# Kernel optimization log

Hardware: AMD Instinct MI355X
Metric: run time of the kernel (lower is better)

## Reference

```python
import jax, jax.numpy as jnp
import numpy as np

N = 32768        # nodes
E = 524288       # edges (avg degree 16)
F_NODE = 64      # NODE_FEATURE_DIM
H = 128          # GNN_HIDDEN
F_EDGE = 32      # EDGE_FEATURE_DIM
L = 3            # GNN_LAYERS
D = 256          # D_MODEL
B = 64           # graphs per batch
MAXN = N // B    # 512 nodes per graph (equal-size for static to_dense_batch)


def setup_inputs() -> dict:
    key = jax.random.key(0)
    ks = jax.random.split(key, 10)
    p = lambda k, shape: jax.random.normal(k, shape, jnp.float32) * 0.02
    return {
        "x": jax.random.normal(ks[0], (N, F_NODE), jnp.float32),
        "edge_attr": jax.random.normal(ks[1], (E, F_EDGE), jnp.float32),
        "node_emb_w": p(ks[2], (F_NODE, H)), "node_emb_b": jnp.zeros((H,), jnp.float32),
        "msg_w1": p(ks[3], (L, 2 * H + F_EDGE, 2 * H)), "msg_b1": jnp.zeros((L, 2 * H), jnp.float32),
        "msg_w2": p(ks[4], (L, 2 * H, H)), "msg_b2": jnp.zeros((L, H), jnp.float32),
        "upd_w": p(ks[5], (L, 2 * H, H)), "upd_b": jnp.zeros((L, H), jnp.float32),
        "upd_ln_g": jnp.ones((L, H), jnp.float32), "upd_ln_b": jnp.zeros((L, H), jnp.float32),
        "norm_g": jnp.ones((L, H), jnp.float32), "norm_b": jnp.zeros((L, H), jnp.float32),
        "proj_w": p(ks[6], (H, D)), "proj_b": jnp.zeros((D,), jnp.float32),
        "edge_index": jax.random.randint(ks[7], (2, E), 0, N),
        "batch": jnp.arange(N, dtype=jnp.int32) // MAXN,  # sorted, 64 graphs of 512
    }


def layer_norm(x, g, b, eps=1e-5):
    m = x.mean(-1, keepdims=True)
    v = ((x - m) ** 2).mean(-1, keepdims=True)
    return (x - m) * jax.lax.rsqrt(v + eps) * g + b


def reference(x, edge_attr, node_emb_w, node_emb_b, msg_w1, msg_b1, msg_w2, msg_b2,
              upd_w, upd_b, upd_ln_g, upd_ln_b, norm_g, norm_b, proj_w, proj_b,
              edge_index, batch):
    src, dst = edge_index[0], edge_index[1]  # PyG: x_j = x[src], x_i = x[dst]
    h = x @ node_emb_w + node_emb_b          # [N, H]
    n_layers = msg_w1.shape[0]
    for l in range(n_layers):
        # message: gather -> concat -> MLP (dropout inactive at eval)
        m = jnp.concatenate([h[dst], h[src], edge_attr], axis=-1)  # [E, 2H+Fe]
        m = jax.nn.relu(m @ msg_w1[l] + msg_b1[l])
        m = m @ msg_w2[l] + msg_b2[l]                               # [E, H]
        # aggregate: scatter-add over destination nodes
        aggr = jax.ops.segment_sum(m, dst, num_segments=h.shape[0])  # [N, H]
        # update: concat -> Linear -> ReLU -> LayerNorm
        u = jnp.concatenate([h, aggr], axis=-1) @ upd_w[l] + upd_b[l]
        u = layer_norm(jax.nn.relu(u), upd_ln_g[l], upd_ln_b[l])
        # residual + outer LayerNorm
        h = layer_norm(h + u, norm_g[l], norm_b[l])
    # to_dense_batch (batch sorted, equal-size graphs -> static [B, MAXN])
    n = h.shape[0]
    counts = jax.ops.segment_sum(jnp.ones((n,), jnp.int32), batch, num_segments=B)
    starts = jnp.concatenate([jnp.zeros((1,), jnp.int32), jnp.cumsum(counts)[:-1]])
    pos = jnp.arange(n, dtype=jnp.int32) - starts[batch]
    dense = jnp.zeros((B, MAXN, h.shape[-1]), h.dtype).at[batch, pos].set(h)
    mask = jnp.zeros((B, MAXN), bool).at[batch, pos].set(True)
    return dense @ proj_w + proj_b, mask
```

## Files before the change

### kernel.cpp

```cpp
#include <hip/hip_runtime.h>

#define NN 32768
#define NE 524288

typedef __attribute__((ext_vector_type(8))) short bf16x8;
typedef __attribute__((ext_vector_type(4))) float f32x4;

__device__ __forceinline__ unsigned short f2bf(float f) {
  unsigned int u = __float_as_uint(f);
  unsigned int r = (u + 0x7FFFu + ((u >> 16) & 1u)) >> 16;
  return (unsigned short)r;
}
__device__ __forceinline__ float bf2f(unsigned short s) {
  return __uint_as_float(((unsigned int)s) << 16);
}

__device__ __forceinline__ void lds_fence_wave() {
  asm volatile("s_waitcnt lgkmcnt(0)" ::: "memory");
  __builtin_amdgcn_sched_barrier(0);
}

__device__ __forceinline__ void prep_frag_body(
    const float* __restrict__ W, int row0, int ldw, long lstrW,
    unsigned short* __restrict__ out, int outOff, int outLstr,
    int K, int N, int t, int total) {
  if (t >= total) return;
  int lane = t & 63, fi = t >> 6;
  int FR = (K >> 5) * (N >> 4);
  int l = fi / FR; fi -= l * FR;
  int NT = N >> 4;
  int nt = fi % NT, kc = fi / NT;
  int i = lane & 15, g = lane >> 4;
  const float* base = W + (long)l * lstrW;
  bf16x8 v;
#pragma unroll
  for (int j = 0; j < 8; ++j)
    v[j] = (short)f2bf(base[(long)(row0 + kc * 32 + g * 8 + j) * ldw + nt * 16 + i]);
  reinterpret_cast<bf16x8*>(out)[(long)(l * outLstr + outOff + fi) * 64 + lane] = v;
}

__global__ void prep_all_kernel(const float* __restrict__ emb_w,
                                const float* __restrict__ msg_w1,
                                const float* __restrict__ upd_w,
                                const float* __restrict__ wcomp,
                                const float* __restrict__ proj_w,
                                unsigned short* __restrict__ wembf,
                                unsigned short* __restrict__ w1af,
                                unsigned short* __restrict__ w1bf,
                                unsigned short* __restrict__ w1cf,
                                unsigned short* __restrict__ wupdf,
                                unsigned short* __restrict__ wprojf) {
  int b = blockIdx.x, tid = threadIdx.x;
  if (b < 4)        prep_frag_body(emb_w,  0,   128, 0,     wembf,  0,  16, 64,  128, b * 256 + tid, 1024);
  else if (b < 52)  prep_frag_body(msg_w1, 0,   256, 73728, w1af,   0,  64, 128, 256, (b - 4) * 256 + tid, 12288);
  else if (b < 100) prep_frag_body(msg_w1, 128, 256, 73728, w1bf,   0,  64, 128, 256, (b - 52) * 256 + tid, 12288);
  else if (b < 112) prep_frag_body(msg_w1, 256, 256, 73728, w1cf,   0,  16, 32,  256, (b - 100) * 256 + tid, 3072);
  else if (b < 136) prep_frag_body(upd_w,  0,   128, 32768, wupdf,  0,  96, 128, 128, (b - 112) * 256 + tid, 6144);
  else if (b < 184) prep_frag_body(wcomp,  0,   128, 32768, wupdf,  32, 96, 256, 128, (b - 136) * 256 + tid, 12288);
  else              prep_frag_body(proj_w, 0,   256, 0,     wprojf, 0,  64, 128, 256, (b - 184) * 256 + tid, 4096);
}

__global__ void wcomp_kernel(const float* __restrict__ W2, const float* __restrict__ Wu,
                             const float* __restrict__ b2,
                             float* __restrict__ out, float* __restrict__ c2out) {
  int t = blockIdx.x * 256 + threadIdx.x;
  if (t < 3 * 256 * 128) {
    int c = t & 127, a = (t >> 7) & 255, l = t >> 15;
    const float* w2 = W2 + (long)l * 32768 + a * 128;
    const float* wu = Wu + (long)l * 32768 + 128 * 128 + c;
    float s = 0.f;
#pragma unroll 8
    for (int j = 0; j < 128; ++j) s += w2[j] * wu[j * 128];
    out[t] = s;
  } else {
    int t2 = t - 3 * 256 * 128;
    if (t2 < 3 * 128) {
      int c = t2 & 127, l = t2 >> 7;
      const float* bb = b2 + l * 128;
      const float* wu = Wu + (long)l * 32768 + 128 * 128 + c;
      float s = 0.f;
#pragma unroll 8
      for (int j = 0; j < 128; ++j) s += bb[j] * wu[j * 128];
      c2out[t2] = s;
    }
  }
}

__global__ void hist_kernel(const int* __restrict__ eidx, int* __restrict__ deg) {
  int t = blockIdx.x * 256 + threadIdx.x;
  if (t < NE) atomicAdd(&deg[eidx[NE + t]], 1);
}

__global__ void scan_kernel(const int* __restrict__ deg, int* __restrict__ cursor,
                            float* __restrict__ degf) {
  __shared__ int lds[1024];
  int t = threadIdx.x;
  int vals[32];
  int s = 0;
#pragma unroll
  for (int j = 0; j < 32; ++j) {
    int d = deg[t * 32 + j];
    vals[j] = d; s += d;
    degf[t * 32 + j] = (float)d;
  }
  lds[t] = s;
  __syncthreads();
  for (int off = 1; off < 1024; off <<= 1) {
    int tmp = 0;
    if (t >= off) tmp = lds[t - off];
    __syncthreads();
    lds[t] += tmp;
    __syncthreads();
  }
  int run = lds[t] - s;
#pragma unroll
  for (int j = 0; j < 32; ++j) { cursor[t * 32 + j] = run; run += vals[j]; }
}

__global__ void scatter_kernel(const int* __restrict__ eidx, const float* __restrict__ ea,
                               int* __restrict__ cursor,
                               int* __restrict__ dsts, int* __restrict__ srcs,
                               unsigned short* __restrict__ ea_s) {
  int t = blockIdx.x * 256 + threadIdx.x;
  if (t >= NE) return;
  int d = eidx[NE + t], s = eidx[t];
  int pos = atomicAdd(&cursor[d], 1);
  dsts[pos] = d;
  srcs[pos] = s;
  const float4* ep = reinterpret_cast<const float4*>(ea + (long)t * 32);
  unsigned short* op = ea_s + (long)pos * 32;
#pragma unroll
  for (int q = 0; q < 4; ++q) {
    float4 f0 = ep[2 * q], f1 = ep[2 * q + 1];
    bf16x8 v;
    v[0] = (short)f2bf(f0.x); v[1] = (short)f2bf(f0.y);
    v[2] = (short)f2bf(f0.z); v[3] = (short)f2bf(f0.w);
    v[4] = (short)f2bf(f1.x); v[5] = (short)f2bf(f1.y);
    v[6] = (short)f2bf(f1.z); v[7] = (short)f2bf(f1.w);
    *reinterpret_cast<bf16x8*>(op + q * 8) = v;
  }
}

__global__ __launch_bounds__(256, 2)
void node_emb_kernel(const float* __restrict__ x,
                     const unsigned short* __restrict__ wf,
                     const float* __restrict__ bias,
                     unsigned short* __restrict__ h_bf) {
  int tid = threadIdx.x, lane = tid & 63, w = tid >> 6;
  int i = lane & 15, g = lane >> 4;
  int nbase = blockIdx.x * 64 + w * 16;
  f32x4 zero = {0.f, 0.f, 0.f, 0.f};
  f32x4 acc[8];
#pragma unroll
  for (int nt = 0; nt < 8; ++nt) acc[nt] = zero;
#pragma unroll
  for (int kc = 0; kc < 2; ++kc) {
    const float* xp = x + (nbase + i) * 64 + kc * 32 + g * 8;
    float4 f0 = *reinterpret_cast<const float4*>(xp);
    float4 f1 = *reinterpret_cast<const float4*>(xp + 4);
    bf16x8 af;
    af[0] = (short)f2bf(f0.x); af[1] = (short)f2bf(f0.y);
    af[2] = (short)f2bf(f0.z); af[3] = (short)f2bf(f0.w);
    af[4] = (short)f2bf(f1.x); af[5] = (short)f2bf(f1.y);
    af[6] = (short)f2bf(f1.z); af[7] = (short)f2bf(f1.w);
#pragma unroll
    for (int nt = 0; nt < 8; ++nt) {
      bf16x8 bf = reinterpret_cast<const bf16x8*>(wf)[(kc * 8 + nt) * 64 + lane];
      acc[nt] = __builtin_amdgcn_mfma_f32_16x16x32_bf16(af, bf, acc[nt], 0, 0, 0);
    }
  }
#pragma unroll
  for (int nt = 0; nt < 8; ++nt) {
    int c = nt * 16 + i;
    float b = bias[c];
#pragma unroll
    for (int r = 0; r < 4; ++r) {
      int node = nbase + 4 * g + r;
      h_bf[node * 128 + c] = f2bf(acc[nt][r] + b);
    }
  }
}

__global__ __launch_bounds__(256, 2)
void pq_kernel(const unsigned short* __restrict__ h_bf,
               const unsigned short* __restrict__ wfa,
               const unsigned short* __restrict__ wfb,
               const float* __restrict__ b1,
               unsigned short* __restrict__ P, unsigned short* __restrict__ Q,
               float* __restrict__ haggr) {
  __shared__ unsigned short xpose[64 * 264];
  int tid = threadIdx.x, lane = tid & 63, w = tid >> 6;
  int i = lane & 15, g = lane >> 4;
  int nbase = blockIdx.x * 64 + w * 16;
  {
    const float4 zz = make_float4(0.f, 0.f, 0.f, 0.f);
    float4* hz = reinterpret_cast<float4*>(haggr + (long)blockIdx.x * 64 * 256);
#pragma unroll
    for (int it = 0; it < 16; ++it) hz[tid + 256 * it] = zz;
  }
  f32x4 zero = {0.f, 0.f, 0.f, 0.f};
  f32x4 accP[16], accQ[16];
#pragma unroll
  for (int nt = 0; nt < 16; ++nt) { accP[nt] = zero; accQ[nt] = zero; }
#pragma unroll
  for (int kc = 0; kc < 4; ++kc) {
    bf16x8 af = *reinterpret_cast<const bf16x8*>(h_bf + (nbase + i) * 128 + kc * 32 + g * 8);
#pragma unroll
    for (int nt = 0; nt < 16; ++nt) {
      bf16x8 ba = reinterpret_cast<const bf16x8*>(wfa)[(kc * 16 + nt) * 64 + lane];
      accP[nt] = __builtin_amdgcn_mfma_f32_16x16x32_bf16(af, ba, accP[nt], 0, 0, 0);
      bf16x8 bb = reinterpret_cast<const bf16x8*>(wfb)[(kc * 16 + nt) * 64 + lane];
      accQ[nt] = __builtin_amdgcn_mfma_f32_16x16x32_bf16(af, bb, accQ[nt], 0, 0, 0);
    }
  }
  const int rowBase = blockIdx.x * 64;
#pragma unroll
  for (int nt = 0; nt < 16; ++nt) {
    int c = nt * 16 + i;
    float b = b1[c];
#pragma unroll
    for (int r = 0; r < 4; ++r)
      xpose[(w * 16 + 4 * g + r) * 264 + c] = f2bf(accP[nt][r] + b);
  }
  __syncthreads();
#pragma unroll
  for (int it = 0; it < 8; ++it) {
    int idx = tid + 256 * it;
    int row = idx >> 5, ch8 = (idx & 31) * 8;
    bf16x8 v = *reinterpret_cast<const bf16x8*>(&xpose[row * 264 + ch8]);
    *reinterpret_cast<bf16x8*>(&P[(long)(rowBase + row) * 256 + ch8]) = v;
  }
  __syncthreads();
#pragma unroll
  for (int nt = 0; nt < 16; ++nt) {
    int c = nt * 16 + i;
#pragma unroll
    for (int r = 0; r < 4; ++r)
      xpose[(w * 16 + 4 * g + r) * 264 + c] = f2bf(accQ[nt][r]);
  }
  __syncthreads();
#pragma unroll
  for (int it = 0; it < 8; ++it) {
    int idx = tid + 256 * it;
    int row = idx >> 5, ch8 = (idx & 31) * 8;
    bf16x8 v = *reinterpret_cast<const bf16x8*>(&xpose[row * 264 + ch8]);
    *reinterpret_cast<bf16x8*>(&Q[(long)(rowBase + row) * 256 + ch8]) = v;
  }
}

#define RP 264
__global__ __launch_bounds__(128, 4)
void edge_kernel10(const unsigned short* __restrict__ P,
                   const unsigned short* __restrict__ Q,
                   const int* __restrict__ dsts, const int* __restrict__ srcs,
                   const unsigned short* __restrict__ ea_s,
                   const unsigned short* __restrict__ w1cf,
                   float* __restrict__ haggr) {
  __shared__ unsigned short R[32 * RP];
  __shared__ float xch[2][256];
  const int tid = threadIdx.x;
  const int lane = tid & 63, w = tid >> 6;
  const int i = lane & 15, g = lane >> 4;
  const int bid = blockIdx.x;
  const int swz = (bid & 7) * 2048 + (bid >> 3);
  const int p0 = swz * 32;
  const int kb = w * 16;

  int d16 = dsts[p0 + kb + (lane & 15)];
  int s16 = srcs[p0 + kb + (lane & 15)];
  int dvs[16], svs[16];
#pragma unroll
  for (int k = 0; k < 16; ++k) {
    dvs[k] = __builtin_amdgcn_readlane(d16, k);
    svs[k] = __builtin_amdgcn_readlane(s16, k);
  }

  const int c4 = lane * 4;
  ushort4 qv[16];
#pragma unroll
  for (int k = 0; k < 16; ++k)
    qv[k] = *reinterpret_cast<const ushort4*>(Q + (long)svs[k] * 256 + c4);
  ushort4 pv0 = *reinterpret_cast<const ushort4*>(P + (long)dvs[0] * 256 + c4);

  {
    bf16x8 bfrag = *reinterpret_cast<const bf16x8*>(ea_s + (long)(p0 + kb + i) * 32 + g * 8);
    f32x4 zero = {0.f, 0.f, 0.f, 0.f};
    f32x4 acc[16];
#pragma unroll
    for (int m = 0; m < 16; ++m) acc[m] = zero;
#pragma unroll
    for (int m = 0; m < 16; ++m) {
      bf16x8 afrag = reinterpret_cast<const bf16x8*>(w1cf)[m * 64 + lane];
      acc[m] = __builtin_amdgcn_mfma_f32_16x16x32_bf16(afrag, bfrag, acc[m], 0, 0, 0);
    }
#pragma unroll
    for (int m = 0; m < 16; ++m) {
      union { unsigned short s[4]; unsigned long long u; } pk;
#pragma unroll
      for (int r = 0; r < 4; ++r) pk.s[r] = f2bf(acc[m][r]);
      *reinterpret_cast<unsigned long long*>(&R[(kb + i) * RP + m * 16 + 4 * g]) = pk.u;
    }
  }

  float pf[4];
  pf[0] = bf2f(pv0.x); pf[1] = bf2f(pv0.y); pf[2] = bf2f(pv0.z); pf[3] = bf2f(pv0.w);
  int dvPrev = dvs[0];

  lds_fence_wave();

  float acc4[4] = {0.f, 0.f, 0.f, 0.f};
#pragma unroll
  for (int k = 0; k < 16; ++k) {
    int dv = dvs[k];
    if (dv != dvPrev) {
      *reinterpret_cast<float4*>(&xch[w][c4]) = make_float4(acc4[0], acc4[1], acc4[2], acc4[3]);
      lds_fence_wave();
      float* hp = haggr + (long)dvPrev * 256;
#pragma unroll
      for (int j = 0; j < 4; ++j) atomicAdd(hp + lane + 64 * j, xch[w][lane + 64 * j]);
      acc4[0] = acc4[1] = acc4[2] = acc4[3] = 0.f;
      ushort4 pv = *reinterpret_cast<const ushort4*>(P + (long)dv * 256 + c4);
      pf[0] = bf2f(pv.x); pf[1] = bf2f(pv.y); pf[2] = bf2f(pv.z); pf[3] = bf2f(pv.w);
      dvPrev = dv;
    }
    ushort4 rv = *reinterpret_cast<const ushort4*>(&R[(kb + k) * RP + c4]);
    float v0 = pf[0] + bf2f(qv[k].x) + bf2f(rv.x);
    float v1 = pf[1] + bf2f(qv[k].y) + bf2f(rv.y);
    float v2 = pf[2] + bf2f(qv[k].z) + bf2f(rv.z);
    float v3 = pf[3] + bf2f(qv[k].w) + bf2f(rv.w);
    acc4[0] += v0 > 0.f ? v0 : 0.f;
    acc4[1] += v1 > 0.f ? v1 : 0.f;
    acc4[2] += v2 > 0.f ? v2 : 0.f;
    acc4[3] += v3 > 0.f ? v3 : 0.f;
  }
  {
    *reinterpret_cast<float4*>(&xch[w][c4]) = make_float4(acc4[0], acc4[1], acc4[2], acc4[3]);
    lds_fence_wave();
    float* hp = haggr + (long)dvPrev * 256;
#pragma unroll
    for (int j = 0; j < 4; ++j) atomicAdd(hp + lane + 64 * j, xch[w][lane + 64 * j]);
  }
}

__global__ __launch_bounds__(256, 2)
void upd_kernel2(const unsigned short* __restrict__ h_bf_in,
                 const float* __restrict__ haggr,
                 const float* __restrict__ degf,
                 const unsigned short* __restrict__ wf,
                 const float* __restrict__ ub, const float* __restrict__ c2,
                 const float* __restrict__ g1, const float* __restrict__ be1,
                 const float* __restrict__ g2, const float* __restrict__ be2,
                 unsigned short* __restrict__ h_bf_out) {
  int tid = threadIdx.x, lane = tid & 63, w = tid >> 6;
  int i = lane & 15, g = lane >> 4;
  int nbase = blockIdx.x * 64 + w * 16;
  f32x4 zero = {0.f, 0.f, 0.f, 0.f};
  f32x4 acc[8];
#pragma unroll
  for (int nt = 0; nt < 8; ++nt) acc[nt] = zero;
#pragma unroll
  for (int kc = 0; kc < 12; ++kc) {
    bf16x8 af;
    if (kc < 4) {
      af = *reinterpret_cast<const bf16x8*>(h_bf_in + (nbase + i) * 128 + kc * 32 + g * 8);
    } else {
      const float* ap = haggr + (long)(nbase + i) * 256 + (kc - 4) * 32 + g * 8;
      float4 f0 = *reinterpret_cast<const float4*>(ap);
      float4 f1 = *reinterpret_cast<const float4*>(ap + 4);
      af[0] = (short)f2bf(f0.x); af[1] = (short)f2bf(f0.y);
      af[2] = (short)f2bf(f0.z); af[3] = (short)f2bf(f0.w);
      af[4] = (short)f2bf(f1.x); af[5] = (short)f2bf(f1.y);
      af[6] = (short)f2bf(f1.z); af[7] = (short)f2bf(f1.w);
    }
#pragma unroll
    for (int nt = 0; nt < 8; ++nt) {
      bf16x8 bf = reinterpret_cast<const bf16x8*>(wf)[(kc * 8 + nt) * 64 + lane];
      acc[nt] = __builtin_amdgcn_mfma_f32_16x16x32_bf16(af, bf, acc[nt], 0, 0, 0);
    }
  }
  float vv[8][4];
#pragma unroll
  for (int nt = 0; nt < 8; ++nt) {
    int c = nt * 16 + i;
    float b = ub[c], cc = c2[c];
#pragma unroll
    for (int r = 0; r < 4; ++r) {
      int node = nbase + 4 * g + r;
      float t = acc[nt][r] + b + degf[node] * cc;
      vv[nt][r] = t > 0.f ? t : 0.f;
    }
  }
#pragma unroll
  for (int r = 0; r < 4; ++r) {
    float s = 0.f, s2 = 0.f;
#pragma unroll
    for (int nt = 0; nt < 8; ++nt) { s += vv[nt][r]; s2 += vv[nt][r] * vv[nt][r]; }
#pragma unroll
    for (int mk = 1; mk < 16; mk <<= 1) { s += __shfl_xor(s, mk, 64); s2 += __shfl_xor(s2, mk, 64); }
    float mean = s * (1.f / 128.f);
    float var = s2 * (1.f / 128.f) - mean * mean;
    float inv = rsqrtf(var + 1e-5f);
    int node = nbase + 4 * g + r;
    float tv[8];
    float sb = 0.f, sb2 = 0.f;
#pragma unroll
    for (int nt = 0; nt < 8; ++nt) {
      int c = nt * 16 + i;
      float u = (vv[nt][r] - mean) * inv * g1[c] + be1[c];
      float t = bf2f(h_bf_in[node * 128 + c]) + u;
      tv[nt] = t;
      sb += t; sb2 += t * t;
    }
#pragma unroll
    for (int mk = 1; mk < 16; mk <<= 1) { sb += __shfl_xor(sb, mk, 64); sb2 += __shfl_xor(sb2, mk, 64); }
    float mean2 = sb * (1.f / 128.f);
    float var2 = sb2 * (1.f / 128.f) - mean2 * mean2;
    float inv2 = rsqrtf(var2 + 1e-5f);
#pragma unroll
    for (int nt = 0; nt < 8; ++nt) {
      int c = nt * 16 + i;
      float o = (tv[nt] - mean2) * inv2 * g2[c] + be2[c];
      h_bf_out[node * 128 + c] = f2bf(o);
    }
  }
}

__global__ __launch_bounds__(256, 2)
void proj_kernel(const unsigned short* __restrict__ h_bf,
                 const unsigned short* __restrict__ wf,
                 const float* __restrict__ bias,
                 float* __restrict__ out, float* __restrict__ mask) {
  int tid = threadIdx.x, lane = tid & 63, w = tid >> 6;
  int i = lane & 15, g = lane >> 4;
  int nbase = blockIdx.x * 64 + w * 16;
  if (tid < 64) mask[blockIdx.x * 64 + tid] = 1.0f;
  f32x4 zero = {0.f, 0.f, 0.f, 0.f};
  f32x4 acc[16];
#pragma unroll
  for (int nt = 0; nt < 16; ++nt) acc[nt] = zero;
#pragma unroll
  for (int kc = 0; kc < 4; ++kc) {
    bf16x8 af = *reinterpret_cast<const bf16x8*>(h_bf + (nbase + i) * 128 + kc * 32 + g * 8);
#pragma unroll
    for (int nt = 0; nt < 16; ++nt) {
      bf16x8 bf = reinterpret_cast<const bf16x8*>(wf)[(kc * 16 + nt) * 64 + lane];
      acc[nt] = __builtin_amdgcn_mfma_f32_16x16x32_bf16(af, bf, acc[nt], 0, 0, 0);
    }
  }
#pragma unroll
  for (int nt = 0; nt < 16; ++nt) {
    int c = nt * 16 + i;
    float b = bias[c];
#pragma unroll
    for (int r = 0; r < 4; ++r) {
      int node = nbase + 4 * g + r;
      out[(long)node * 256 + c] = acc[nt][r] + b;
    }
  }
}

extern "C" void kernel_launch(void* const* d_in, const int* in_sizes, int n_in,
                              void* d_out, int out_size, void* d_ws, size_t ws_size,
                              hipStream_t stream) {
  const float* x      = (const float*)d_in[0];
  const float* ea     = (const float*)d_in[1];
  const float* emb_w  = (const float*)d_in[2];
  const float* emb_b  = (const float*)d_in[3];
  const float* msg_w1 = (const float*)d_in[4];
  const float* msg_b1 = (const float*)d_in[5];
  const float* msg_w2 = (const float*)d_in[6];
  const float* msg_b2 = (const float*)d_in[7];
  const float* upd_w  = (const float*)d_in[8];
  const float* upd_b  = (const float*)d_in[9];
  const float* uln_g  = (const float*)d_in[10];
  const float* uln_b  = (const float*)d_in[11];
  const float* nrm_g  = (const float*)d_in[12];
  const float* nrm_b  = (const float*)d_in[13];
  const float* proj_w = (const float*)d_in[14];
  const float* proj_b = (const float*)d_in[15];
  const int*   eidx   = (const int*)d_in[16];

  char* ws = (char*)d_ws;
  size_t off = 0;
  auto take = [&](size_t b) { char* p = ws + off; off = (off + b + 255) & ~(size_t)255; return p; };
  unsigned short* h_bf  = (unsigned short*)take((size_t)NN * 128 * 2);
  unsigned short* Pb    = (unsigned short*)take((size_t)NN * 256 * 2);
  unsigned short* Qb    = (unsigned short*)take((size_t)NN * 256 * 2);
  float*          haggr = (float*)take((size_t)NN * 256 * 4);
  unsigned short* ea_s  = (unsigned short*)take((size_t)NE * 32 * 2);
  int*            dsts  = (int*)take((size_t)NE * 4);
  int*            srcs  = (int*)take((size_t)NE * 4);
  int*            deg   = (int*)take((size_t)NN * 4);
  int*            cursor= (int*)take((size_t)NN * 4);
  float*          degf  = (float*)take((size_t)NN * 4);
  float*          wcomp = (float*)take((size_t)3 * 256 * 128 * 4);
  float*          c2b   = (float*)take((size_t)3 * 128 * 4);
  unsigned short* wembf = (unsigned short*)take((size_t)16 * 64 * 8 * 2);
  unsigned short* w1af  = (unsigned short*)take((size_t)3 * 64 * 64 * 8 * 2);
  unsigned short* w1bf  = (unsigned short*)take((size_t)3 * 64 * 64 * 8 * 2);
  unsigned short* w1cf  = (unsigned short*)take((size_t)3 * 16 * 64 * 8 * 2);
  unsigned short* wupdf = (unsigned short*)take((size_t)3 * 96 * 64 * 8 * 2);
  unsigned short* wprojf= (unsigned short*)take((size_t)64 * 64 * 8 * 2);
  (void)ws_size; (void)n_in; (void)in_sizes;

  hipMemsetAsync(deg, 0, (size_t)NN * 4, stream);
  hist_kernel<<<2048, 256, 0, stream>>>(eidx, deg);
  scan_kernel<<<1, 1024, 0, stream>>>(deg, cursor, degf);
  scatter_kernel<<<2048, 256, 0, stream>>>(eidx, ea, cursor, dsts, srcs, ea_s);
  wcomp_kernel<<<386, 256, 0, stream>>>(msg_w2, upd_w, msg_b2, wcomp, c2b);
  prep_all_kernel<<<200, 256, 0, stream>>>(emb_w, msg_w1, upd_w, wcomp, proj_w,
                                           wembf, w1af, w1bf, w1cf, wupdf, wprojf);

  node_emb_kernel<<<512, 256, 0, stream>>>(x, wembf, emb_b, h_bf);

  for (int l = 0; l < 3; ++l) {
    pq_kernel<<<512, 256, 0, stream>>>(h_bf, w1af + (size_t)l * 32768, w1bf + (size_t)l * 32768,
                                       msg_b1 + l * 256, Pb, Qb, haggr);
    edge_kernel10<<<NE / 32, 128, 0, stream>>>(Pb, Qb, dsts, srcs, ea_s,
                                               w1cf + (size_t)l * 8192, haggr);
    upd_kernel2<<<512, 256, 0, stream>>>(h_bf, haggr, degf,
                                         wupdf + (size_t)l * 49152, upd_b + l * 128,
                                         c2b + l * 128,
                                         uln_g + l * 128, uln_b + l * 128,
                                         nrm_g + l * 128, nrm_b + l * 128, h_bf);
  }

  proj_kernel<<<512, 256, 0, stream>>>(h_bf, wprojf, proj_b, (float*)d_out,
                                       (float*)d_out + (size_t)NN * 256);
}
```

Measured before the change: 447.5 us.

## Process 32 edges per single-wave block and fill sorted dst array deterministically

The edge kernel now uses one 64-thread wave per block handling all 32 edges, instead of two waves of 16. This roughly halves the atomic flushes to haggr for destination runs that previously spanned the two waves, at the cost of more registers (32 gathered Q rows held at once) and lower wave count per block. Separately, the sorted destination array is now written by a per-node fill kernel rather than inside the atomic scatter. This removes one scattered store per edge but leaves a divergent per-node loop.

```diff
diff --git a/kernel.cpp b/kernel.cpp
--- a/kernel.cpp
+++ b/kernel.cpp
@@ -117,15 +117,22 @@
   for (int j = 0; j < 32; ++j) { cursor[t * 32 + j] = run; run += vals[j]; }
 }
 
+__global__ void fill_dsts_kernel(const int* __restrict__ deg, const int* __restrict__ cursor,
+                                 int* __restrict__ dsts) {
+  int n = blockIdx.x * 256 + threadIdx.x;
+  if (n >= NN) return;
+  int st = cursor[n], de = deg[n];
+  for (int j = 0; j < de; ++j) dsts[st + j] = n;
+}
+
 __global__ void scatter_kernel(const int* __restrict__ eidx, const float* __restrict__ ea,
                                int* __restrict__ cursor,
-                               int* __restrict__ dsts, int* __restrict__ srcs,
+                               int* __restrict__ srcs,
                                unsigned short* __restrict__ ea_s) {
   int t = blockIdx.x * 256 + threadIdx.x;
   if (t >= NE) return;
   int d = eidx[NE + t], s = eidx[t];
   int pos = atomicAdd(&cursor[d], 1);
-  dsts[pos] = d;
   srcs[pos] = s;
   const float4* ep = reinterpret_cast<const float4*>(ea + (long)t * 32);
   unsigned short* op = ea_s + (long)pos * 32;
@@ -249,41 +256,39 @@
 }
 
 #define RP 264
-__global__ __launch_bounds__(128, 4)
-void edge_kernel10(const unsigned short* __restrict__ P,
+__global__ __launch_bounds__(64, 2)
+void edge_kernel11(const unsigned short* __restrict__ P,
                    const unsigned short* __restrict__ Q,
                    const int* __restrict__ dsts, const int* __restrict__ srcs,
                    const unsigned short* __restrict__ ea_s,
                    const unsigned short* __restrict__ w1cf,
                    float* __restrict__ haggr) {
   __shared__ unsigned short R[32 * RP];
-  __shared__ float xch[2][256];
-  const int tid = threadIdx.x;
-  const int lane = tid & 63, w = tid >> 6;
+  __shared__ float xch[256];
+  const int lane = threadIdx.x & 63;
   const int i = lane & 15, g = lane >> 4;
   const int bid = blockIdx.x;
   const int swz = (bid & 7) * 2048 + (bid >> 3);
   const int p0 = swz * 32;
-  const int kb = w * 16;
-
-  int d16 = dsts[p0 + kb + (lane & 15)];
-  int s16 = srcs[p0 + kb + (lane & 15)];
-  int dvs[16], svs[16];
-#pragma unroll
-  for (int k = 0; k < 16; ++k) {
-    dvs[k] = __builtin_amdgcn_readlane(d16, k);
-    svs[k] = __builtin_amdgcn_readlane(s16, k);
-  }
+
+  int d32 = dsts[p0 + (lane & 31)];
+  int s32 = srcs[p0 + (lane & 31)];
 
   const int c4 = lane * 4;
-  ushort4 qv[16];
-#pragma unroll
-  for (int k = 0; k < 16; ++k)
-    qv[k] = *reinterpret_cast<const ushort4*>(Q + (long)svs[k] * 256 + c4);
+  ushort4 qv[32];
+#pragma unroll
+  for (int k = 0; k < 32; ++k) {
+    int sv = __builtin_amdgcn_readlane(s32, k);
+    qv[k] = *reinterpret_cast<const ushort4*>(Q + (long)sv * 256 + c4);
+  }
+  int dvs[32];
+#pragma unroll
+  for (int k = 0; k < 32; ++k) dvs[k] = __builtin_amdgcn_readlane(d32, k);
   ushort4 pv0 = *reinterpret_cast<const ushort4*>(P + (long)dvs[0] * 256 + c4);
 
-  {
-    bf16x8 bfrag = *reinterpret_cast<const bf16x8*>(ea_s + (long)(p0 + kb + i) * 32 + g * 8);
+#pragma unroll
+  for (int half = 0; half < 2; ++half) {
+    bf16x8 bfrag = *reinterpret_cast<const bf16x8*>(ea_s + (long)(p0 + half * 16 + i) * 32 + g * 8);
     f32x4 zero = {0.f, 0.f, 0.f, 0.f};
     f32x4 acc[16];
 #pragma unroll
@@ -298,7 +303,7 @@
       union { unsigned short s[4]; unsigned long long u; } pk;
 #pragma unroll
       for (int r = 0; r < 4; ++r) pk.s[r] = f2bf(acc[m][r]);
-      *reinterpret_cast<unsigned long long*>(&R[(kb + i) * RP + m * 16 + 4 * g]) = pk.u;
+      *reinterpret_cast<unsigned long long*>(&R[(half * 16 + i) * RP + m * 16 + 4 * g]) = pk.u;
     }
   }
 
@@ -310,20 +315,20 @@
 
   float acc4[4] = {0.f, 0.f, 0.f, 0.f};
 #pragma unroll
-  for (int k = 0; k < 16; ++k) {
+  for (int k = 0; k < 32; ++k) {
     int dv = dvs[k];
     if (dv != dvPrev) {
-      *reinterpret_cast<float4*>(&xch[w][c4]) = make_float4(acc4[0], acc4[1], acc4[2], acc4[3]);
+      *reinterpret_cast<float4*>(&xch[c4]) = make_float4(acc4[0], acc4[1], acc4[2], acc4[3]);
       lds_fence_wave();
       float* hp = haggr + (long)dvPrev * 256;
 #pragma unroll
-      for (int j = 0; j < 4; ++j) atomicAdd(hp + lane + 64 * j, xch[w][lane + 64 * j]);
+      for (int j = 0; j < 4; ++j) atomicAdd(hp + lane + 64 * j, xch[lane + 64 * j]);
       acc4[0] = acc4[1] = acc4[2] = acc4[3] = 0.f;
       ushort4 pv = *reinterpret_cast<const ushort4*>(P + (long)dv * 256 + c4);
       pf[0] = bf2f(pv.x); pf[1] = bf2f(pv.y); pf[2] = bf2f(pv.z); pf[3] = bf2f(pv.w);
       dvPrev = dv;
     }
-    ushort4 rv = *reinterpret_cast<const ushort4*>(&R[(kb + k) * RP + c4]);
+    ushort4 rv = *reinterpret_cast<const ushort4*>(&R[k * RP + c4]);
     float v0 = pf[0] + bf2f(qv[k].x) + bf2f(rv.x);
     float v1 = pf[1] + bf2f(qv[k].y) + bf2f(rv.y);
     float v2 = pf[2] + bf2f(qv[k].z) + bf2f(rv.z);
@@ -334,11 +339,11 @@
     acc4[3] += v3 > 0.f ? v3 : 0.f;
   }
   {
-    *reinterpret_cast<float4*>(&xch[w][c4]) = make_float4(acc4[0], acc4[1], acc4[2], acc4[3]);
+    *reinterpret_cast<float4*>(&xch[c4]) = make_float4(acc4[0], acc4[1], acc4[2], acc4[3]);
     lds_fence_wave();
     float* hp = haggr + (long)dvPrev * 256;
 #pragma unroll
-    for (int j = 0; j < 4; ++j) atomicAdd(hp + lane + 64 * j, xch[w][lane + 64 * j]);
+    for (int j = 0; j < 4; ++j) atomicAdd(hp + lane + 64 * j, xch[lane + 64 * j]);
   }
 }
 
@@ -506,7 +511,8 @@
   hipMemsetAsync(deg, 0, (size_t)NN * 4, stream);
   hist_kernel<<<2048, 256, 0, stream>>>(eidx, deg);
   scan_kernel<<<1, 1024, 0, stream>>>(deg, cursor, degf);
-  scatter_kernel<<<2048, 256, 0, stream>>>(eidx, ea, cursor, dsts, srcs, ea_s);
+  fill_dsts_kernel<<<128, 256, 0, stream>>>(deg, cursor, dsts);
+  scatter_kernel<<<2048, 256, 0, stream>>>(eidx, ea, cursor, srcs, ea_s);
   wcomp_kernel<<<386, 256, 0, stream>>>(msg_w2, upd_w, msg_b2, wcomp, c2b);
   prep_all_kernel<<<200, 256, 0, stream>>>(emb_w, msg_w1, upd_w, wcomp, proj_w,
                                            wembf, w1af, w1bf, w1cf, wupdf, wprojf);
@@ -516,8 +522,8 @@
   for (int l = 0; l < 3; ++l) {
     pq_kernel<<<512, 256, 0, stream>>>(h_bf, w1af + (size_t)l * 32768, w1bf + (size_t)l * 32768,
                                        msg_b1 + l * 256, Pb, Qb, haggr);
-    edge_kernel10<<<NE / 32, 128, 0, stream>>>(Pb, Qb, dsts, srcs, ea_s,
-                                               w1cf + (size_t)l * 8192, haggr);
+    edge_kernel11<<<NE / 32, 64, 0, stream>>>(Pb, Qb, dsts, srcs, ea_s,
+                                              w1cf + (size_t)l * 8192, haggr);
     upd_kernel2<<<512, 256, 0, stream>>>(h_bf, haggr, degf,
                                          wupdf + (size_t)l * 49152, upd_b + l * 128,
                                          c2b + l * 128,
```

Result: slower. 460.2 us (+2.8%).
